# Optimization experiments

Hardware: AMD Instinct MI355X
Metric: run time of the kernel (lower is better)

## Reference

```python
import jax, jax.numpy as jnp
import numpy as np

B, H, K, V, MUL = 512, 1024, 256, 512, 4
EPS = 1e-6
WRITE_RATE = 0.1
FORGET_RATE = 0.02


def _rms_norm(x):
    # parameter-free RMS norm (matches the module-level rms_norm helper)
    ms = jnp.mean(x.astype(jnp.float32) ** 2, axis=-1, keepdims=True)
    return (x.astype(jnp.float32) * jax.lax.rsqrt(ms + EPS)).astype(x.dtype)


def setup_inputs() -> dict:
    key = jax.random.key(0)
    ks = jax.random.split(key, 16)
    std = 1.0 / np.sqrt(H)
    f32 = jnp.float32
    return {
        "x": jax.random.normal(ks[0], (B, H), f32),
        "memory": jax.random.normal(ks[1], (B, K, V), f32) * 0.1,
        "valid": jnp.ones((B,), jnp.bool_),
        "w_read_key": jax.random.normal(ks[2], (H, K), f32) * std,
        "w_write_key": jax.random.normal(ks[3], (H, K), f32) * std,
        "w_write_value": jax.random.normal(ks[4], (H, V), f32) * std,
        "w_read_proj": jax.random.normal(ks[5], (V, H), f32) * std,
        "w_write_gate": jax.random.normal(ks[6], (H, 1), f32) * std,
        "b_write_gate": jnp.zeros((1,), f32),
        "w_forget_gate": jax.random.normal(ks[7], (H, 1), f32) * std,
        "b_forget_gate": jnp.zeros((1,), f32),
        "scale1": jnp.ones((H,), f32),
        "scale2": jnp.ones((H,), f32),
        "scale3": jnp.ones((H,), f32),
        "w_fc1": jax.random.normal(ks[8], (H, MUL * H), f32) * std,
        "b_fc1": jnp.zeros((MUL * H,), f32),
        "w_fc2": jax.random.normal(ks[9], (MUL * H, H), f32) * (1.0 / np.sqrt(MUL * H)),
        "b_fc2": jnp.zeros((H,), f32),
        "gamma1": jnp.ones((H,), f32) * 0.1,
        "gamma2": jnp.ones((H,), f32) * 0.1,
    }


def reference(x, memory, valid, w_read_key, w_write_key, w_write_value,
              w_read_proj, w_write_gate, b_write_gate, w_forget_gate,
              b_forget_gate, scale1, scale2, scale3, w_fc1, b_fc1,
              w_fc2, b_fc2, gamma1, gamma2):
    inv_sqrt_k = jax.lax.rsqrt(jnp.asarray(K, jnp.float32))
    memory_f32 = memory.astype(jnp.float32)

    # --- memory read ---
    h = _rms_norm(x) * scale1                                   # RMSNorm (norm1)
    read_key = _rms_norm(h @ w_read_key) * inv_sqrt_k           # [B, K]
    read_value = jnp.einsum('bkv,bk->bv', memory_f32, read_key) # [B, V]
    x = x + gamma1 * (read_value @ w_read_proj)

    # --- MLP ---
    mlp_in = _rms_norm(x) * scale2                              # RMSNorm (norm2)
    x = x + gamma2 * (jax.nn.silu(mlp_in @ w_fc1 + b_fc1) @ w_fc2 + b_fc2)

    # --- memory write (delta-rule style outer-product update) ---
    w = _rms_norm(x) * scale3                                   # RMSNorm (norm3)
    write_key = _rms_norm(w @ w_write_key) * inv_sqrt_k         # [B, K]
    write_value = jnp.tanh(w @ w_write_value)                   # [B, V]
    value_hat = jnp.einsum('bkv,bk->bv', memory_f32, write_key) # [B, V]
    err = jnp.clip(write_value - value_hat, -1.0, 1.0)
    eta = jax.nn.sigmoid(w @ w_write_gate + b_write_gate) * WRITE_RATE     # [B, 1]
    forget = jax.nn.sigmoid(w @ w_forget_gate + b_forget_gate) * FORGET_RATE
    update = jnp.einsum('bk,bv->bkv', write_key, err)           # [B, K, V]
    new_memory = (1.0 - forget[:, :, None]) * memory_f32 + eta[:, :, None] * update
    new_memory = jnp.clip(new_memory, -10.0, 10.0)

    valid_f = valid.astype(jnp.float32)[:, None, None]
    final_memory = valid_f * new_memory + (1.0 - valid_f) * memory_f32
    return (x.astype(jnp.float32), final_memory)
```

## Files before the change

### kernel.cpp

```cpp
#include <hip/hip_runtime.h>
#include <math.h>

constexpr int B_ = 512;
constexpr int H_ = 1024;
constexpr int K_ = 256;
constexpr int V_ = 512;
constexpr int F_ = 4096;

typedef __attribute__((ext_vector_type(8))) short bf16x8;
typedef __attribute__((ext_vector_type(4))) float f32x4;

#define GLD16(gp, lp)                                                   \
  __builtin_amdgcn_global_load_lds(                                     \
      (const __attribute__((address_space(1))) void*)(gp),              \
      (__attribute__((address_space(3))) void*)(lp), 16, 0, 0)

static __device__ __forceinline__ unsigned short f2bf(float f) {
  union { float f; unsigned int u; } a; a.f = f;
  unsigned int u = a.u;
  return (unsigned short)((u + 0x7FFFu + ((u >> 16) & 1u)) >> 16);
}

static __device__ __forceinline__ float block_sum256(float v, float* sbuf) {
#pragma unroll
  for (int o = 32; o > 0; o >>= 1) v += __shfl_down(v, o, 64);
  const int w = threadIdx.x >> 6;
  __syncthreads();
  if ((threadIdx.x & 63) == 0) sbuf[w] = v;
  __syncthreads();
  return sbuf[0] + sbuf[1] + sbuf[2] + sbuf[3];
}

static __device__ __forceinline__ float block_sum512(float v, float* sbuf) {
#pragma unroll
  for (int o = 32; o > 0; o >>= 1) v += __shfl_down(v, o, 64);
  const int w = threadIdx.x >> 6;
  __syncthreads();
  if ((threadIdx.x & 63) == 0) sbuf[w] = v;
  __syncthreads();
  float s = 0.f;
#pragma unroll
  for (int i = 0; i < 8; ++i) s += sbuf[i];
  return s;
}

struct TJob { const float* src; unsigned short* dst; int R, C, cb, blk0; };
struct TArgs { TJob j[6]; };

__global__ __launch_bounds__(256) void prep_kernel(
    TArgs args, const float* __restrict__ x, const float* __restrict__ scale,
    unsigned short* __restrict__ h1, int tblocks) {
  __shared__ unsigned short t16[64][68];
  __shared__ float sbuf[4];
  const int id = blockIdx.x;
  const int tid = threadIdx.x;
  if (id >= tblocks) {
    const int b = id - tblocks;
    const float* xr = x + ((size_t)b << 10);
    float loc[4]; float ss = 0.f;
#pragma unroll
    for (int it = 0; it < 4; ++it) { float v = xr[(it << 8) + tid]; loc[it] = v; ss += v * v; }
    ss = block_sum256(ss, sbuf);
    const float r = rsqrtf(ss * (1.f / 1024.f) + 1e-6f);
    unsigned short* orow = h1 + ((size_t)b << 10);
#pragma unroll
    for (int it = 0; it < 4; ++it) { const int j = (it << 8) + tid; orow[j] = f2bf(loc[it] * r * scale[j]); }
    return;
  }
  int ji = 0;
#pragma unroll
  for (int i = 1; i < 6; ++i) if (id >= args.j[i].blk0) ji = i;
  const TJob J = args.j[ji];
  const int lb = id - J.blk0;
  const int bx = lb % J.cb, by = lb / J.cb;
  const int c0 = bx << 6, r0 = by << 6;
  const int lr = tid >> 4, lc = (tid & 15) << 2;
#pragma unroll
  for (int i = 0; i < 4; ++i) {
    const int row = (i << 4) + lr;
    const f32x4 v = *(const f32x4*)&J.src[(size_t)(r0 + row) * J.C + c0 + lc];
    ushort4 u;
    u.x = f2bf(v.x); u.y = f2bf(v.y); u.z = f2bf(v.z); u.w = f2bf(v.w);
    *(ushort4*)&t16[row][lc] = u;
  }
  __syncthreads();
  const int oc = tid >> 5, j = tid & 31;
#pragma unroll
  for (int i = 0; i < 8; ++i) {
    const int c = (i << 3) + oc;
    const unsigned lo = t16[2 * j][c], hi = t16[2 * j + 1][c];
    *(unsigned*)&J.dst[(size_t)(c0 + c) * J.R + r0 + 2 * j] = lo | (hi << 16);
  }
}

template <int BN, bool SILU>
__global__ __launch_bounds__(256) void gemm2(
    const unsigned short* __restrict__ A, const unsigned short* __restrict__ BT,
    float* __restrict__ Cf, unsigned short* __restrict__ Cb,
    const float* __restrict__ bias, int M, int N, int K, int Ksub) {
  __shared__ unsigned short lsa[2][64 * 64];
  __shared__ unsigned short lsb[2][BN * 64];
  const int tid = threadIdx.x;
  const int m0 = blockIdx.y << 6, n0 = blockIdx.x * BN;
  const int kbeg = blockIdx.z * Ksub;
  const int w = tid >> 6, l = tid & 63;
  const int l15 = l & 15, lg = l >> 4;
  const int wm = (w >> 1) * 32, wn = (w & 1) * (BN / 2);
  constexpr int NF = BN / 32;
  f32x4 acc[2][NF] = {};

  const int sr = l >> 3;
  const int sc = ((l & 7) ^ sr) * 8;
  const int srow = w * 8 + sr;
  const unsigned short* ga0 = A + (size_t)(m0 + srow) * K + sc;
  const unsigned short* gb0 = BT + (size_t)(n0 + srow) * K + sc;
  const int rx = l15 & 7;

  auto STAGE = [&](int buf, int k0) {
#pragma unroll
    for (int c = 0; c < 2; ++c)
      GLD16(ga0 + (size_t)(c * 32) * K + k0, &lsa[buf][c * 2048 + w * 512]);
#pragma unroll
    for (int c = 0; c < NF; ++c)
      GLD16(gb0 + (size_t)(c * 32) * K + k0, &lsb[buf][c * 2048 + w * 512]);
  };

  const int nt = Ksub >> 6;
  STAGE(0, kbeg);
  __builtin_amdgcn_sched_barrier(0);
  int cur = 0;
  for (int t = 0; t < nt; ++t) {
    if (t + 1 < nt) {
      STAGE(cur ^ 1, kbeg + ((t + 1) << 6));
      __builtin_amdgcn_sched_barrier(0);
      if constexpr (NF == 2) {
        asm volatile("s_waitcnt vmcnt(4)" ::: "memory");
      } else {
        asm volatile("s_waitcnt vmcnt(6)" ::: "memory");
      }
    } else {
      asm volatile("s_waitcnt vmcnt(0)" ::: "memory");
    }
    __builtin_amdgcn_sched_barrier(0);
    __builtin_amdgcn_s_barrier();
    __builtin_amdgcn_sched_barrier(0);
    const unsigned short* la = lsa[cur];
    const unsigned short* lb = lsb[cur];
    bf16x8 af[2][2], bv[2][NF];
#pragma unroll
    for (int kh = 0; kh < 2; ++kh) {
      const int ch = ((kh * 4 + lg) ^ rx) * 8;
#pragma unroll
      for (int mf = 0; mf < 2; ++mf)
        af[kh][mf] = *(const bf16x8*)&la[(wm + mf * 16 + l15) * 64 + ch];
#pragma unroll
      for (int nf = 0; nf < NF; ++nf)
        bv[kh][nf] = *(const bf16x8*)&lb[(wn + nf * 16 + l15) * 64 + ch];
    }
#pragma unroll
    for (int kh = 0; kh < 2; ++kh)
#pragma unroll
      for (int mf = 0; mf < 2; ++mf)
#pragma unroll
        for (int nf = 0; nf < NF; ++nf)
          acc[mf][nf] = __builtin_amdgcn_mfma_f32_16x16x32_bf16(
              af[kh][mf], bv[kh][nf], acc[mf][nf], 0, 0, 0);
    asm volatile("s_waitcnt lgkmcnt(0)" ::: "memory");
    __builtin_amdgcn_sched_barrier(0);
    __builtin_amdgcn_s_barrier();
    __builtin_amdgcn_sched_barrier(0);
    cur ^= 1;
  }

  if constexpr (SILU) {
#pragma unroll
    for (int mf = 0; mf < 2; ++mf)
#pragma unroll
      for (int nf = 0; nf < NF; ++nf) {
        const int col = n0 + wn + nf * 16 + l15;
        const float bi = bias[col];
#pragma unroll
        for (int i = 0; i < 4; ++i) {
          const int row = m0 + wm + mf * 16 + (lg << 2) + i;
          const float z = acc[mf][nf][i] + bi;
          Cb[(size_t)row * N + col] = f2bf(z / (1.f + expf(-z)));
        }
      }
  } else {
    float* Cz = Cf + (size_t)blockIdx.z * M * N;
#pragma unroll
    for (int mf = 0; mf < 2; ++mf)
#pragma unroll
      for (int nf = 0; nf < NF; ++nf) {
        const int r = m0 + wm + mf * 16 + (lg << 2);
        const int c = n0 + wn + nf * 16 + l15;
        float* cp = Cz + (size_t)r * N + c;
#pragma unroll
        for (int i = 0; i < 4; ++i) cp[(size_t)i * N] = acc[mf][nf][i];
      }
  }
}

__global__ __launch_bounds__(512) void read_einsum(
    const float* __restrict__ mem, const float* __restrict__ rk_pre,
    unsigned short* __restrict__ rv) {
  __shared__ float sbuf[8];
  __shared__ float lrk[256];
  __shared__ float part[8][256];
  const int tid = threadIdx.x;
  const int b = blockIdx.x >> 1;
  const int v0 = (blockIdx.x & 1) << 8;
  {
    constexpr size_t PS = (size_t)B_ * K_;
    float v = 0.f;
    if (tid < 256) {
#pragma unroll
      for (int z = 0; z < 4; ++z) v += rk_pre[z * PS + ((size_t)b << 8) + tid];
    }
    const float ss = block_sum512(v * v, sbuf);
    if (tid < 256) lrk[tid] = v * rsqrtf(ss * (1.f / 256.f) + 1e-6f) * 0.0625f;
  }
  __syncthreads();
  const int w = tid >> 6, l = tid & 63;
  const float* base = mem + ((size_t)b << 17) + v0 + (l << 2);
  f32x4 a = {0.f, 0.f, 0.f, 0.f};
#pragma unroll 8
  for (int kk = 0; kk < 32; ++kk) {
    const int k = (w << 5) + kk;
    const f32x4 m4 = *(const f32x4*)(base + ((size_t)k << 9));
    const float s = lrk[k];
    a.x += s * m4.x; a.y += s * m4.y; a.z += s * m4.z; a.w += s * m4.w;
  }
  *(f32x4*)&part[w][l << 2] = a;
  __syncthreads();
  if (tid < 256) {
    float s = 0.f;
#pragma unroll
    for (int g = 0; g < 8; ++g) s += part[g][tid];
    rv[((size_t)b << 9) + v0 + tid] = f2bf(s);
  }
}

__global__ __launch_bounds__(256) void add1_norm2(
    const float* __restrict__ x, const float* __restrict__ proj,
    const float* __restrict__ gamma1, const float* __restrict__ scale2,
    float* __restrict__ x1, unsigned short* __restrict__ h2) {
  __shared__ float sbuf[4];
  const int b = blockIdx.x, tid = threadIdx.x;
  const size_t ro = (size_t)b << 10;
  constexpr size_t PS = (size_t)B_ * H_;
  float loc[4]; float ss = 0.f;
#pragma unroll
  for (int it = 0; it < 4; ++it) {
    const int j = (it << 8) + tid;
    const float v = x[ro + j] + gamma1[j] * (proj[ro + j] + proj[PS + ro + j]);
    x1[ro + j] = v; loc[it] = v; ss += v * v;
  }
  ss = block_sum256(ss, sbuf);
  const float r = rsqrtf(ss * (1.f / 1024.f) + 1e-6f);
#pragma unroll
  for (int it = 0; it < 4; ++it) { const int j = (it << 8) + tid; h2[ro + j] = f2bf(loc[it] * r * scale2[j]); }
}

__global__ __launch_bounds__(256) void add2_norm3(
    const float* __restrict__ x1, const float* __restrict__ fc2p,
    const float* __restrict__ gamma2, const float* __restrict__ bias2,
    const float* __restrict__ scale3, const float* __restrict__ wgate,
    const float* __restrict__ bgate, const float* __restrict__ wforget,
    const float* __restrict__ bforget, float* __restrict__ xout,
    unsigned short* __restrict__ w3, float* __restrict__ eta, float* __restrict__ fg) {
  __shared__ float sbuf[4];
  const int b = blockIdx.x, tid = threadIdx.x;
  const size_t ro = (size_t)b << 10;
  constexpr size_t PS = (size_t)B_ * H_;
  float loc[4]; float ss = 0.f;
#pragma unroll
  for (int it = 0; it < 4; ++it) {
    const int j = (it << 8) + tid;
    float acc = bias2[j];
#pragma unroll
    for (int z = 0; z < 4; ++z) acc += fc2p[z * PS + ro + j];
    const float v = x1[ro + j] + gamma2[j] * acc;
    xout[ro + j] = v; loc[it] = v; ss += v * v;
  }
  ss = block_sum256(ss, sbuf);
  const float r = rsqrtf(ss * (1.f / 1024.f) + 1e-6f);
  float dg = 0.f, df = 0.f;
#pragma unroll
  for (int it = 0; it < 4; ++it) {
    const int j = (it << 8) + tid;
    const float w = loc[it] * r * scale3[j];
    w3[ro + j] = f2bf(w);
    dg += w * wgate[j]; df += w * wforget[j];
  }
  dg = block_sum256(dg, sbuf);
  df = block_sum256(df, sbuf);
  if (tid == 0) {
    eta[b] = 0.1f / (1.f + expf(-(dg + bgate[0])));
    fg[b] = 0.02f / (1.f + expf(-(df + bforget[0])));
  }
}

__global__ __launch_bounds__(512) void write_update(
    const float* __restrict__ mem, const float* __restrict__ wkvp,
    const float* __restrict__ eta, const float* __restrict__ fg,
    const unsigned char* __restrict__ valid, float* __restrict__ outm) {
  __shared__ float sbuf[8];
  __shared__ float lwk[256];
  __shared__ float part[8][256];
  __shared__ float lerr[256];
  const int tid = threadIdx.x;
  const int b = blockIdx.x >> 1;
  const int v0 = (blockIdx.x & 1) << 8;
  constexpr size_t PS = (size_t)B_ * 768;
  {
    float v = 0.f;
    if (tid < 256) v = wkvp[(size_t)b * 768 + tid] + wkvp[PS + (size_t)b * 768 + tid];
    const float ss = block_sum512(v * v, sbuf);
    if (tid < 256) lwk[tid] = v * rsqrtf(ss * (1.f / 256.f) + 1e-6f) * 0.0625f;
  }
  __syncthreads();
  const int w = tid >> 6, l = tid & 63;
  const float* mb = mem + ((size_t)b << 17) + v0 + (l << 2);
  {
    f32x4 a = {0.f, 0.f, 0.f, 0.f};
#pragma unroll 8
    for (int kk = 0; kk < 32; ++kk) {
      const int k = (w << 5) + kk;
      const f32x4 m4 = *(const f32x4*)(mb + ((size_t)k << 9));
      const float s = lwk[k];
      a.x += s * m4.x; a.y += s * m4.y; a.z += s * m4.z; a.w += s * m4.w;
    }
    *(f32x4*)&part[w][l << 2] = a;
  }
  __syncthreads();
  if (tid < 256) {
    float vh = 0.f;
#pragma unroll
    for (int g = 0; g < 8; ++g) vh += part[g][tid];
    const size_t wvo = (size_t)b * 768 + 256 + v0 + tid;
    const float wv = tanhf(wkvp[wvo] + wkvp[PS + wvo]);
    lerr[tid] = fminf(1.f, fmaxf(-1.f, wv - vh));
  }
  __syncthreads();
  const float et = eta[b], fo = fg[b];
  const float omf = 1.f - fo;
  const bool vb = valid[b] != 0;
  const f32x4 e4 = *(const f32x4*)&lerr[l << 2];
  float* ob = outm + ((size_t)b << 17) + v0 + (l << 2);
#pragma unroll 8
  for (int kk = 0; kk < 32; ++kk) {
    const int k = (w << 5) + kk;
    const float wke = lwk[k] * et;
    const f32x4 m4 = *(const f32x4*)(mb + ((size_t)k << 9));
    f32x4 r;
    r.x = fminf(10.f, fmaxf(-10.f, omf * m4.x + wke * e4.x));
    r.y = fminf(10.f, fmaxf(-10.f, omf * m4.y + wke * e4.y));
    r.z = fminf(10.f, fmaxf(-10.f, omf * m4.z + wke * e4.z));
    r.w = fminf(10.f, fmaxf(-10.f, omf * m4.w + wke * e4.w));
    if (!vb) { r.x = m4.x; r.y = m4.y; r.z = m4.z; r.w = m4.w; }
    __builtin_nontemporal_store(r, (f32x4*)(ob + ((size_t)k << 9)));
  }
}

extern "C" void kernel_launch(void* const* d_in, const int* in_sizes, int n_in,
                              void* d_out, int out_size, void* d_ws, size_t ws_size,
                              hipStream_t stream) {
  const float* x = (const float*)d_in[0];
  const float* mem = (const float*)d_in[1];
  const unsigned char* valid = (const unsigned char*)d_in[2];
  const float* w_rk = (const float*)d_in[3];
  const float* w_wk = (const float*)d_in[4];
  const float* w_wv = (const float*)d_in[5];
  const float* w_rp = (const float*)d_in[6];
  const float* w_wg = (const float*)d_in[7];
  const float* b_wg = (const float*)d_in[8];
  const float* w_fg = (const float*)d_in[9];
  const float* b_fg = (const float*)d_in[10];
  const float* scale1 = (const float*)d_in[11];
  const float* scale2 = (const float*)d_in[12];
  const float* scale3 = (const float*)d_in[13];
  const float* w_fc1 = (const float*)d_in[14];
  const float* b_fc1 = (const float*)d_in[15];
  const float* w_fc2 = (const float*)d_in[16];
  const float* b_fc2 = (const float*)d_in[17];
  const float* gamma1 = (const float*)d_in[18];
  const float* gamma2 = (const float*)d_in[19];

  char* ws = (char*)d_ws;
  size_t off = 0;
  auto alloc = [&](size_t bytes) -> void* {
    void* p = (void*)(ws + off);
    off = (off + bytes + 255) & ~(size_t)255;
    return p;
  };

  unsigned short* wT_rk = (unsigned short*)alloc((size_t)K_ * H_ * 2);
  unsigned short* wT_wkv = (unsigned short*)alloc((size_t)768 * H_ * 2);
  unsigned short* wT_rp = (unsigned short*)alloc((size_t)H_ * V_ * 2);
  unsigned short* wT_f1 = (unsigned short*)alloc((size_t)F_ * H_ * 2);
  unsigned short* wT_f2 = (unsigned short*)alloc((size_t)H_ * F_ * 2);
  unsigned short* h1 = (unsigned short*)alloc((size_t)B_ * H_ * 2);
  float* rk_pre = (float*)alloc((size_t)4 * B_ * K_ * 4);
  unsigned short* rv = (unsigned short*)alloc((size_t)B_ * V_ * 2);
  float* projp = (float*)alloc((size_t)2 * B_ * H_ * 4);
  float* x1 = (float*)alloc((size_t)B_ * H_ * 4);
  unsigned short* h2 = (unsigned short*)alloc((size_t)B_ * H_ * 2);
  unsigned short* ybf = (unsigned short*)alloc((size_t)B_ * F_ * 2);
  float* fc2p = (float*)alloc((size_t)4 * B_ * H_ * 4);
  unsigned short* w3 = (unsigned short*)alloc((size_t)B_ * H_ * 2);
  float* wkvp = (float*)alloc((size_t)2 * B_ * 768 * 4);
  float* eta = (float*)alloc((size_t)B_ * 4);
  float* fg = (float*)alloc((size_t)B_ * 4);

  float* xout = (float*)d_out;
  float* outm = (float*)d_out + (size_t)B_ * H_;

  TArgs ta;
  int blk = 0;
  auto setj = [&](int i, const float* s, unsigned short* d, int R, int C) {
    ta.j[i] = {s, d, R, C, C / 64, blk};
    blk += (R / 64) * (C / 64);
  };
  setj(0, w_rk, wT_rk, H_, K_);
  setj(1, w_wk, wT_wkv, H_, K_);
  setj(2, w_wv, wT_wkv + (size_t)K_ * H_, H_, V_);
  setj(3, w_rp, wT_rp, V_, H_);
  setj(4, w_fc1, wT_f1, H_, F_);
  setj(5, w_fc2, wT_f2, F_, H_);
  prep_kernel<<<blk + B_, 256, 0, stream>>>(ta, x, scale1, h1, blk);

  gemm2<64, false><<<dim3(K_ / 64, B_ / 64, 4), 256, 0, stream>>>(
      h1, wT_rk, rk_pre, nullptr, nullptr, B_, K_, H_, H_ / 4);
  read_einsum<<<B_ * 2, 512, 0, stream>>>(mem, rk_pre, rv);
  gemm2<64, false><<<dim3(H_ / 64, B_ / 64, 2), 256, 0, stream>>>(
      rv, wT_rp, projp, nullptr, nullptr, B_, H_, V_, V_ / 2);
  add1_norm2<<<B_, 256, 0, stream>>>(x, projp, gamma1, scale2, x1, h2);

  gemm2<128, true><<<dim3(F_ / 128, B_ / 64), 256, 0, stream>>>(
      h2, wT_f1, nullptr, ybf, b_fc1, B_, F_, H_, H_);
  gemm2<128, false><<<dim3(H_ / 128, B_ / 64, 4), 256, 0, stream>>>(
      ybf, wT_f2, fc2p, nullptr, nullptr, B_, H_, F_, F_ / 4);
  add2_norm3<<<B_, 256, 0, stream>>>(x1, fc2p, gamma2, b_fc2, scale3, w_wg, b_wg,
                                     w_fg, b_fg, xout, w3, eta, fg);

  gemm2<64, false><<<dim3(768 / 64, B_ / 64, 2), 256, 0, stream>>>(
      w3, wT_wkv, wkvp, nullptr, nullptr, B_, 768, H_, H_ / 2);
  write_update<<<B_ * 2, 512, 0, stream>>>(mem, wkvp, eta, fg, valid, outm);
}
```

Baseline: 247.0 us.

## Keep memory tile in registers across read and update passes in write_update

The write-update kernel now splits each batch row into four 128-column blocks and has each thread cache its 16 float4 memory values in registers. The update pass reuses them instead of re-reading memory from global. This removes the second full read of the large memory tensor. The cost is higher register pressure, handled with an occupancy hint in the launch bounds, and a finer grid with more partial-sum groups.

```diff
diff --git a/kernel.cpp b/kernel.cpp
--- a/kernel.cpp
+++ b/kernel.cpp
@@ -301,17 +301,17 @@
   }
 }
 
-__global__ __launch_bounds__(512) void write_update(
+__global__ __launch_bounds__(512, 4) void write_update(
     const float* __restrict__ mem, const float* __restrict__ wkvp,
     const float* __restrict__ eta, const float* __restrict__ fg,
     const unsigned char* __restrict__ valid, float* __restrict__ outm) {
   __shared__ float sbuf[8];
   __shared__ float lwk[256];
-  __shared__ float part[8][256];
-  __shared__ float lerr[256];
+  __shared__ f32x4 part[16][32];
+  __shared__ float lerr[128];
   const int tid = threadIdx.x;
-  const int b = blockIdx.x >> 1;
-  const int v0 = (blockIdx.x & 1) << 8;
+  const int b = blockIdx.x >> 2;
+  const int v0 = (blockIdx.x & 3) << 7;
   constexpr size_t PS = (size_t)B_ * 768;
   {
     float v = 0.f;
@@ -321,23 +321,27 @@
   }
   __syncthreads();
   const int w = tid >> 6, l = tid & 63;
-  const float* mb = mem + ((size_t)b << 17) + v0 + (l << 2);
+  const int g = (w << 1) + (l >> 5);
+  const int c4 = l & 31;
+  const float* mb = mem + ((size_t)b << 17) + v0 + (c4 << 2);
+  f32x4 buf[16];
   {
     f32x4 a = {0.f, 0.f, 0.f, 0.f};
-#pragma unroll 8
-    for (int kk = 0; kk < 32; ++kk) {
-      const int k = (w << 5) + kk;
-      const f32x4 m4 = *(const f32x4*)(mb + ((size_t)k << 9));
+#pragma unroll
+    for (int i = 0; i < 16; ++i) {
+      const int k = (i << 4) + g;
+      buf[i] = *(const f32x4*)(mb + ((size_t)k << 9));
       const float s = lwk[k];
-      a.x += s * m4.x; a.y += s * m4.y; a.z += s * m4.z; a.w += s * m4.w;
+      a.x += s * buf[i].x; a.y += s * buf[i].y;
+      a.z += s * buf[i].z; a.w += s * buf[i].w;
     }
-    *(f32x4*)&part[w][l << 2] = a;
-  }
-  __syncthreads();
-  if (tid < 256) {
+    part[g][c4] = a;
+  }
+  __syncthreads();
+  if (tid < 128) {
     float vh = 0.f;
 #pragma unroll
-    for (int g = 0; g < 8; ++g) vh += part[g][tid];
+    for (int gg = 0; gg < 16; ++gg) vh += part[gg][tid >> 2][tid & 3];
     const size_t wvo = (size_t)b * 768 + 256 + v0 + tid;
     const float wv = tanhf(wkvp[wvo] + wkvp[PS + wvo]);
     lerr[tid] = fminf(1.f, fmaxf(-1.f, wv - vh));
@@ -346,19 +350,18 @@
   const float et = eta[b], fo = fg[b];
   const float omf = 1.f - fo;
   const bool vb = valid[b] != 0;
-  const f32x4 e4 = *(const f32x4*)&lerr[l << 2];
-  float* ob = outm + ((size_t)b << 17) + v0 + (l << 2);
-#pragma unroll 8
-  for (int kk = 0; kk < 32; ++kk) {
-    const int k = (w << 5) + kk;
+  const f32x4 e4 = *(const f32x4*)&lerr[c4 << 2];
+  float* ob = outm + ((size_t)b << 17) + v0 + (c4 << 2);
+#pragma unroll
+  for (int i = 0; i < 16; ++i) {
+    const int k = (i << 4) + g;
     const float wke = lwk[k] * et;
-    const f32x4 m4 = *(const f32x4*)(mb + ((size_t)k << 9));
     f32x4 r;
-    r.x = fminf(10.f, fmaxf(-10.f, omf * m4.x + wke * e4.x));
-    r.y = fminf(10.f, fmaxf(-10.f, omf * m4.y + wke * e4.y));
-    r.z = fminf(10.f, fmaxf(-10.f, omf * m4.z + wke * e4.z));
-    r.w = fminf(10.f, fmaxf(-10.f, omf * m4.w + wke * e4.w));
-    if (!vb) { r.x = m4.x; r.y = m4.y; r.z = m4.z; r.w = m4.w; }
+    r.x = fminf(10.f, fmaxf(-10.f, omf * buf[i].x + wke * e4.x));
+    r.y = fminf(10.f, fmaxf(-10.f, omf * buf[i].y + wke * e4.y));
+    r.z = fminf(10.f, fmaxf(-10.f, omf * buf[i].z + wke * e4.z));
+    r.w = fminf(10.f, fmaxf(-10.f, omf * buf[i].w + wke * e4.w));
+    if (!vb) r = buf[i];
     __builtin_nontemporal_store(r, (f32x4*)(ob + ((size_t)k << 9)));
   }
 }
@@ -446,5 +449,5 @@
 
   gemm2<64, false><<<dim3(768 / 64, B_ / 64, 2), 256, 0, stream>>>(
       w3, wT_wkv, wkvp, nullptr, nullptr, B_, 768, H_, H_ / 2);
-  write_update<<<B_ * 2, 512, 0, stream>>>(mem, wkvp, eta, fg, valid, outm);
-}
+  write_update<<<B_ * 4, 512, 0, stream>>>(mem, wkvp, eta, fg, valid, outm);
+}
```

Result: faster. 224.5 us (-9.1%).
